# Kernel optimization log

Measured on AMD Instinct MI355X. Metric: run time of the kernel, lower is better.

## Reference

```python
import jax, jax.numpy as jnp
import numpy as np

EPS = 1e-5  # BatchNorm eps


def _bn_relu(x, g, b, m, v):
    # inference-mode BatchNorm2d over channel axis 1, then ReLU
    inv = g / jnp.sqrt(v + EPS)
    return jax.nn.relu(x * inv[None, :, None, None] + (b - m * inv)[None, :, None, None])


def setup_inputs() -> dict:
    key = jax.random.key(0)
    ks = jax.random.split(key, 16)
    B, C, N, K = 8, 64, 16384, 16
    mlp = (128, 64, 64)
    inp = {
        "src_xyz": jax.random.normal(ks[0], (B, 3, N, K), jnp.float32),
        "tgt_xyz": jax.random.normal(ks[1], (B, 3, N), jnp.float32),
        "feature": jax.random.normal(ks[2], (B, C, N, K), jnp.float32),
    }
    prev = C + 4  # use_relation adds diff_xyz(3) + distance(1)
    i = 3
    for li, co in enumerate(mlp, 1):
        scale = (6.0 / (prev + co)) ** 0.5  # xavier_uniform
        inp[f"W{li}"] = jax.random.uniform(ks[i], (co, prev), jnp.float32, -scale, scale)
        inp[f"g{li}"] = jnp.ones((co,), jnp.float32)
        inp[f"b{li}"] = jnp.zeros((co,), jnp.float32)
        inp[f"m{li}"] = jnp.zeros((co,), jnp.float32)
        inp[f"v{li}"] = jnp.ones((co,), jnp.float32)
        prev = co
        i += 1
    return inp


def reference(src_xyz, tgt_xyz, feature,
              W1, g1, b1, m1, v1,
              W2, g2, b2, m2, v2,
              W3, g3, b3, m3, v3):
    d = 3  # NOTE: original code slices the NEIGHBOR dim to :3 (faithful quirk)
    diff = src_xyz[:, :, :, :d] - tgt_xyz[:, :, :, None]      # (B,3,N,3)
    dist = jnp.sum(diff * diff, axis=1, keepdims=True)        # (B,1,N,3)
    x = jnp.concatenate([feature[:, :, :, :d], diff, dist], axis=1)  # (B,C+4,N,3)
    for (W, g, b, m, v) in ((W1, g1, b1, m1, v1), (W2, g2, b2, m2, v2), (W3, g3, b3, m3, v3)):
        x = jnp.einsum('oc,bcnk->bonk', W, x)  # 1x1 conv (shared MLP)
        x = _bn_relu(x, g, b, m, v)
    return jnp.sum(x, axis=3)  # reduction='sum' over neighbor dim -> (B,64,N)
```

## Files before the change

kernel.cpp:

```cpp
#include <hip/hip_runtime.h>


typedef __attribute__((ext_vector_type(8))) short short8v;
typedef __attribute__((ext_vector_type(4))) float f32x4;

#define BN_EPS 1e-5f

__device__ __forceinline__ unsigned short f2bf(float f) {
    union { float f; unsigned u; } U; U.f = f;
    unsigned r = U.u + 0x7FFFu + ((U.u >> 16) & 1u);
    return (unsigned short)(r >> 16);
}

union FragU { uint4 u; short8v s; uint2 h[2]; };


__global__ __launch_bounds__(256) void fa_pack(
    const float* __restrict__ W1, const float* __restrict__ g1, const float* __restrict__ b1,
    const float* __restrict__ m1, const float* __restrict__ v1,
    const float* __restrict__ W2, const float* __restrict__ g2, const float* __restrict__ b2,
    const float* __restrict__ m2, const float* __restrict__ v2,
    const float* __restrict__ W3, const float* __restrict__ g3, const float* __restrict__ b3,
    const float* __restrict__ m3, const float* __restrict__ v3,
    char* __restrict__ ws)
{
    const int id = blockIdx.x * 256 + threadIdx.x;
    if (id < 1536) {
        const int lane = id & 63, frag = id >> 6;
        const int ct = frag / 3, ks = frag - 3 * ct;
        const int o  = ct * 16 + (lane & 15);
        const int kb = ks * 32 + (lane >> 4) * 8;
        unsigned short h[8];
        #pragma unroll
        for (int j = 0; j < 8; ++j) {
            const int k = kb + j;
            h[j] = (k < 68) ? f2bf(W1[o * 68 + k]) : (unsigned short)0;
        }
        uint4 pk;
        pk.x = h[0] | (h[1] << 16); pk.y = h[2] | (h[3] << 16);
        pk.z = h[4] | (h[5] << 16); pk.w = h[6] | (h[7] << 16);
        ((uint4*)ws)[id] = pk;
    } else if (id < 2560) {
        const int i2 = id - 1536;
        const int lane = i2 & 63, frag = i2 >> 6;
        const int o  = (frag >> 2) * 16 + (lane & 15);
        const int kb = (frag & 3) * 32 + (lane >> 4) * 8;
        unsigned short h[8];
        #pragma unroll
        for (int j = 0; j < 8; ++j) h[j] = f2bf(W2[o * 128 + kb + j]);
        uint4 pk;
        pk.x = h[0] | (h[1] << 16); pk.y = h[2] | (h[3] << 16);
        pk.z = h[4] | (h[5] << 16); pk.w = h[6] | (h[7] << 16);
        ((uint4*)(ws + 24576))[i2] = pk;
    } else if (id < 3072) {
        const int i3 = id - 2560;
        const int lane = i3 & 63, frag = i3 >> 6;
        const int o  = (frag >> 1) * 16 + (lane & 15);
        const int kb = (frag & 1) * 32 + (lane >> 4) * 8;
        unsigned short h[8];
        #pragma unroll
        for (int j = 0; j < 8; ++j) h[j] = f2bf(W3[o * 64 + kb + j]);
        uint4 pk;
        pk.x = h[0] | (h[1] << 16); pk.y = h[2] | (h[3] << 16);
        pk.z = h[4] | (h[5] << 16); pk.w = h[6] | (h[7] << 16);
        ((uint4*)(ws + 40960))[i3] = pk;
    } else if (id < 3200) {
        const int o = id - 3072;
        const float s = g1[o] * rsqrtf(v1[o] + BN_EPS);
        ((float*)(ws + 49152))[o] = s;
        ((float*)(ws + 49664))[o] = b1[o] - m1[o] * s;
    } else if (id < 3264) {
        const int o = id - 3200;
        const float s = g2[o] * rsqrtf(v2[o] + BN_EPS);
        ((float*)(ws + 50176))[o] = s;
        ((float*)(ws + 50432))[o] = b2[o] - m2[o] * s;
    } else if (id < 3328) {
        const int o = id - 3264;
        const float s = g3[o] * rsqrtf(v3[o] + BN_EPS);
        ((float*)(ws + 50688))[o] = s;
        ((float*)(ws + 50944))[o] = b3[o] - m3[o] * s;
    }
}

__global__ __launch_bounds__(128, 3) void fa_mfma(
    const float* __restrict__ src, const float* __restrict__ tgt,
    const float* __restrict__ feat,
    const char* __restrict__ ws, float* __restrict__ out)
{
    constexpr int N = 16384;
    __shared__ unsigned short SM[96 * 136];
    #define X0V(r, c) SM[(r) * 72 + (c)]
    #define X1V(r, c) SM[(r) * 136 + (c)]

    const int t  = threadIdx.x;
    const int b  = blockIdx.x >> 9;
    const int n0 = (blockIdx.x & 511) << 5;

    {
        const int p  = t & 31;
        const int cg = t >> 5;
        float4 fr[16];
        #pragma unroll
        for (int it = 0; it < 4; ++it) {
            const float* fp = feat + ((size_t)(b * 64 + it * 16 + cg * 4) * N + n0 + p) * 16;
            #pragma unroll
            for (int q = 0; q < 4; ++q)
                fr[it * 4 + q] = *(const float4*)(fp + (size_t)q * N * 16);
        }
        float rs0 = 0, rs1 = 0, rs2 = 0, rt0 = 0, rt1 = 0, rt2 = 0;
        const bool rel = t < 96;
        const int rp = t & 31, rk = t >> 5;
        if (rel) {
            const int n = n0 + rp;
            rs0 = src[((b * 3 + 0) * N + n) * 16 + rk]; rt0 = tgt[(b * 3 + 0) * N + n];
            rs1 = src[((b * 3 + 1) * N + n) * 16 + rk]; rt1 = tgt[(b * 3 + 1) * N + n];
            rs2 = src[((b * 3 + 2) * N + n) * 16 + rk]; rt2 = tgt[(b * 3 + 2) * N + n];
        }
        #pragma unroll
        for (int it = 0; it < 4; ++it) {
            const int c0 = it * 16 + cg * 4;
            const float4 f0 = fr[it * 4 + 0], f1 = fr[it * 4 + 1];
            const float4 f2 = fr[it * 4 + 2], f3 = fr[it * 4 + 3];
            uint2 u0, u1, u2;
            u0.x = f2bf(f0.x) | (f2bf(f1.x) << 16); u0.y = f2bf(f2.x) | (f2bf(f3.x) << 16);
            u1.x = f2bf(f0.y) | (f2bf(f1.y) << 16); u1.y = f2bf(f2.y) | (f2bf(f3.y) << 16);
            u2.x = f2bf(f0.z) | (f2bf(f1.z) << 16); u2.y = f2bf(f2.z) | (f2bf(f3.z) << 16);
            *(uint2*)&X0V(0 * 32 + p, c0) = u0;
            *(uint2*)&X0V(1 * 32 + p, c0) = u1;
            *(uint2*)&X0V(2 * 32 + p, c0) = u2;
        }
        if (rel) {
            const float d0 = rs0 - rt0, d1 = rs1 - rt1, d2 = rs2 - rt2;
            const float ds = d0 * d0 + d1 * d1 + d2 * d2;
            uint2 wr; wr.x = f2bf(d0) | (f2bf(d1) << 16); wr.y = f2bf(d2) | (f2bf(ds) << 16);
            *(uint2*)&X0V(rk * 32 + rp, 64) = wr;
        }
    }
    __syncthreads();

    const int w = t >> 6, lane = t & 63, lo = lane & 15, hi = lane >> 4;

    const uint4*  w1f = (const uint4*)ws;
    const uint4*  w2f = (const uint4*)(ws + 24576);
    const uint4*  w3f = (const uint4*)(ws + 40960);
    const float*  s1w = (const float*)(ws + 49152);
    const float*  t1w = (const float*)(ws + 49664);
    const float*  s2w = (const float*)(ws + 50176);
    const float*  t2w = (const float*)(ws + 50432);
    const float*  s3w = (const float*)(ws + 50688);
    const float*  t3w = (const float*)(ws + 50944);

    short8v a1[3][3];
    #pragma unroll
    for (int k = 0; k < 3; ++k) {
        const int row = k * 32 + w * 16 + lo;
        a1[k][0] = *(const short8v*)&X0V(row, hi * 8);
        a1[k][1] = *(const short8v*)&X0V(row, 32 + hi * 8);
        FragU U; U.u.x = 0; U.u.y = 0; U.u.z = 0; U.u.w = 0;
        if (hi == 0) U.h[0] = *(const uint2*)&X0V(row, 64);
        a1[k][2] = U.s;
    }
    __syncthreads();

    #pragma unroll 2
    for (int ct = 0; ct < 8; ++ct) {
        FragU B0, B1, B2;
        B0.u = w1f[(ct * 3 + 0) * 64 + lane];
        B1.u = w1f[(ct * 3 + 1) * 64 + lane];
        B2.u = w1f[(ct * 3 + 2) * 64 + lane];
        const float sc = s1w[ct * 16 + lo];
        const float tb = t1w[ct * 16 + lo];
        #pragma unroll
        for (int k = 0; k < 3; ++k) {
            f32x4 acc = {0.f, 0.f, 0.f, 0.f};
            acc = __builtin_amdgcn_mfma_f32_16x16x32_bf16(a1[k][0], B0.s, acc, 0, 0, 0);
            acc = __builtin_amdgcn_mfma_f32_16x16x32_bf16(a1[k][1], B1.s, acc, 0, 0, 0);
            acc = __builtin_amdgcn_mfma_f32_16x16x32_bf16(a1[k][2], B2.s, acc, 0, 0, 0);
            const int rb = k * 32 + w * 16 + 4 * hi;
            #pragma unroll
            for (int j = 0; j < 4; ++j) {
                const float y = fmaxf(fmaf(sc, acc[j], tb), 0.f);
                X1V(rb + j, ct * 16 + lo) = f2bf(y);
            }
        }
    }

    short8v a2[3][4];
    #pragma unroll
    for (int k = 0; k < 3; ++k) {
        const int row = k * 32 + w * 16 + lo;
        #pragma unroll
        for (int ks = 0; ks < 4; ++ks)
            a2[k][ks] = *(const short8v*)&X1V(row, ks * 32 + hi * 8);
    }
    __syncthreads();

    #pragma unroll 2
    for (int ct = 0; ct < 4; ++ct) {
        FragU B0, B1, B2, B3;
        B0.u = w2f[(ct * 4 + 0) * 64 + lane];
        B1.u = w2f[(ct * 4 + 1) * 64 + lane];
        B2.u = w2f[(ct * 4 + 2) * 64 + lane];
        B3.u = w2f[(ct * 4 + 3) * 64 + lane];
        const float sc = s2w[ct * 16 + lo];
        const float tb = t2w[ct * 16 + lo];
        #pragma unroll
        for (int k = 0; k < 3; ++k) {
            f32x4 acc = {0.f, 0.f, 0.f, 0.f};
            acc = __builtin_amdgcn_mfma_f32_16x16x32_bf16(a2[k][0], B0.s, acc, 0, 0, 0);
            acc = __builtin_amdgcn_mfma_f32_16x16x32_bf16(a2[k][1], B1.s, acc, 0, 0, 0);
            acc = __builtin_amdgcn_mfma_f32_16x16x32_bf16(a2[k][2], B2.s, acc, 0, 0, 0);
            acc = __builtin_amdgcn_mfma_f32_16x16x32_bf16(a2[k][3], B3.s, acc, 0, 0, 0);
            const int rb = k * 32 + w * 16 + 4 * hi;
            #pragma unroll
            for (int j = 0; j < 4; ++j) {
                const float y = fmaxf(fmaf(sc, acc[j], tb), 0.f);
                X0V(rb + j, ct * 16 + lo) = f2bf(y);
            }
        }
    }

    short8v a3[3][2];
    #pragma unroll
    for (int k = 0; k < 3; ++k) {
        const int row = k * 32 + w * 16 + lo;
        a3[k][0] = *(const short8v*)&X0V(row, hi * 8);
        a3[k][1] = *(const short8v*)&X0V(row, 32 + hi * 8);
    }
    #pragma unroll 2
    for (int ct = 0; ct < 4; ++ct) {
        FragU B0, B1;
        B0.u = w3f[(ct * 2 + 0) * 64 + lane];
        B1.u = w3f[(ct * 2 + 1) * 64 + lane];
        const float sc = s3w[ct * 16 + lo];
        const float tb = t3w[ct * 16 + lo];
        f32x4 acc0 = {0.f, 0.f, 0.f, 0.f};
        f32x4 acc1 = {0.f, 0.f, 0.f, 0.f};
        f32x4 acc2 = {0.f, 0.f, 0.f, 0.f};
        acc0 = __builtin_amdgcn_mfma_f32_16x16x32_bf16(a3[0][0], B0.s, acc0, 0, 0, 0);
        acc0 = __builtin_amdgcn_mfma_f32_16x16x32_bf16(a3[0][1], B1.s, acc0, 0, 0, 0);
        acc1 = __builtin_amdgcn_mfma_f32_16x16x32_bf16(a3[1][0], B0.s, acc1, 0, 0, 0);
        acc1 = __builtin_amdgcn_mfma_f32_16x16x32_bf16(a3[1][1], B1.s, acc1, 0, 0, 0);
        acc2 = __builtin_amdgcn_mfma_f32_16x16x32_bf16(a3[2][0], B0.s, acc2, 0, 0, 0);
        acc2 = __builtin_amdgcn_mfma_f32_16x16x32_bf16(a3[2][1], B1.s, acc2, 0, 0, 0);
        float4 r;
        float* rp = &r.x;
        #pragma unroll
        for (int j = 0; j < 4; ++j) {
            rp[j] = fmaxf(fmaf(sc, acc0[j], tb), 0.f)
                  + fmaxf(fmaf(sc, acc1[j], tb), 0.f)
                  + fmaxf(fmaf(sc, acc2[j], tb), 0.f);
        }
        float* op = out + (size_t)(b * 64 + ct * 16 + lo) * N + n0 + w * 16 + 4 * hi;
        *(float4*)op = r;
    }
    #undef X0V
    #undef X1V
}

extern "C" void kernel_launch(void* const* d_in, const int* in_sizes, int n_in,
                              void* d_out, int out_size, void* d_ws, size_t ws_size,
                              hipStream_t stream)
{
    const float* src  = (const float*)d_in[0];
    const float* tgt  = (const float*)d_in[1];
    const float* feat = (const float*)d_in[2];
    const float* W1 = (const float*)d_in[3];
    const float* g1 = (const float*)d_in[4];
    const float* b1 = (const float*)d_in[5];
    const float* m1 = (const float*)d_in[6];
    const float* v1 = (const float*)d_in[7];
    const float* W2 = (const float*)d_in[8];
    const float* g2 = (const float*)d_in[9];
    const float* b2 = (const float*)d_in[10];
    const float* m2 = (const float*)d_in[11];
    const float* v2 = (const float*)d_in[12];
    const float* W3 = (const float*)d_in[13];
    const float* g3 = (const float*)d_in[14];
    const float* b3 = (const float*)d_in[15];
    const float* m3 = (const float*)d_in[16];
    const float* v3 = (const float*)d_in[17];
    float* out = (float*)d_out;
    char* ws = (char*)d_ws;

    hipLaunchKernelGGL(fa_pack, dim3(13), dim3(256), 0, stream,
                       W1, g1, b1, m1, v1, W2, g2, b2, m2, v2, W3, g3, b3, m3, v3, ws);
    hipLaunchKernelGGL(fa_mfma, dim3(8 * 512), dim3(128), 0, stream,
                       src, tgt, feat, ws, out);
}
```

Baseline: 136.7 us.

## Process two tiles per block and prefetch the second tile's inputs during MLP compute

Each block now handles two consecutive 32-point tiles and launches half as many blocks. The global loads of feature, src and tgt for the second tile are issued while layers 1 and 2 of the first tile run, then packed into bf16 and written to shared memory after the first tile's layer-3 fragments are read. This is meant to hide global memory latency behind MFMA work. In exchange it uses more registers for the prefetch buffers, which may hurt occupancy under the launch bound of 3, and it halves the grid size.

```diff
diff --git a/kernel.cpp b/kernel.cpp
--- a/kernel.cpp
+++ b/kernel.cpp
@@ -93,28 +93,44 @@
     #define X1V(r, c) SM[(r) * 136 + (c)]
 
     const int t  = threadIdx.x;
-    const int b  = blockIdx.x >> 9;
-    const int n0 = (blockIdx.x & 511) << 5;
+    const int T0 = blockIdx.x * 2;
+    const int b0  = T0 >> 9;
+    const int n00 = (T0 & 511) << 5;
+    const int b1t  = (T0 + 1) >> 9;
+    const int n01 = ((T0 + 1) & 511) << 5;
+
+    const int p  = t & 31;
+    const int cg = t >> 5;
+    const bool rel = t < 96;
+    const int rp = t & 31, rk = t >> 5;
+
+    const int w = t >> 6, lane = t & 63, lo = lane & 15, hi = lane >> 4;
+
+    const uint4*  w1f = (const uint4*)ws;
+    const uint4*  w2f = (const uint4*)(ws + 24576);
+    const uint4*  w3f = (const uint4*)(ws + 40960);
+    const float*  s1w = (const float*)(ws + 49152);
+    const float*  t1w = (const float*)(ws + 49664);
+    const float*  s2w = (const float*)(ws + 50176);
+    const float*  t2w = (const float*)(ws + 50432);
+    const float*  s3w = (const float*)(ws + 50688);
+    const float*  t3w = (const float*)(ws + 50944);
 
     {
-        const int p  = t & 31;
-        const int cg = t >> 5;
         float4 fr[16];
         #pragma unroll
         for (int it = 0; it < 4; ++it) {
-            const float* fp = feat + ((size_t)(b * 64 + it * 16 + cg * 4) * N + n0 + p) * 16;
+            const float* fp = feat + ((size_t)(b0 * 64 + it * 16 + cg * 4) * N + n00 + p) * 16;
             #pragma unroll
             for (int q = 0; q < 4; ++q)
                 fr[it * 4 + q] = *(const float4*)(fp + (size_t)q * N * 16);
         }
         float rs0 = 0, rs1 = 0, rs2 = 0, rt0 = 0, rt1 = 0, rt2 = 0;
-        const bool rel = t < 96;
-        const int rp = t & 31, rk = t >> 5;
         if (rel) {
-            const int n = n0 + rp;
-            rs0 = src[((b * 3 + 0) * N + n) * 16 + rk]; rt0 = tgt[(b * 3 + 0) * N + n];
-            rs1 = src[((b * 3 + 1) * N + n) * 16 + rk]; rt1 = tgt[(b * 3 + 1) * N + n];
-            rs2 = src[((b * 3 + 2) * N + n) * 16 + rk]; rt2 = tgt[(b * 3 + 2) * N + n];
+            const int n = n00 + rp;
+            rs0 = src[((b0 * 3 + 0) * N + n) * 16 + rk]; rt0 = tgt[(b0 * 3 + 0) * N + n];
+            rs1 = src[((b0 * 3 + 1) * N + n) * 16 + rk]; rt1 = tgt[(b0 * 3 + 1) * N + n];
+            rs2 = src[((b0 * 3 + 2) * N + n) * 16 + rk]; rt2 = tgt[(b0 * 3 + 2) * N + n];
         }
         #pragma unroll
         for (int it = 0; it < 4; ++it) {
@@ -138,18 +154,6 @@
     }
     __syncthreads();
 
-    const int w = t >> 6, lane = t & 63, lo = lane & 15, hi = lane >> 4;
-
-    const uint4*  w1f = (const uint4*)ws;
-    const uint4*  w2f = (const uint4*)(ws + 24576);
-    const uint4*  w3f = (const uint4*)(ws + 40960);
-    const float*  s1w = (const float*)(ws + 49152);
-    const float*  t1w = (const float*)(ws + 49664);
-    const float*  s2w = (const float*)(ws + 50176);
-    const float*  t2w = (const float*)(ws + 50432);
-    const float*  s3w = (const float*)(ws + 50688);
-    const float*  t3w = (const float*)(ws + 50944);
-
     short8v a1[3][3];
     #pragma unroll
     for (int k = 0; k < 3; ++k) {
@@ -161,6 +165,22 @@
         a1[k][2] = U.s;
     }
     __syncthreads();
+
+    float4 frA[8];
+    #pragma unroll
+    for (int it = 0; it < 2; ++it) {
+        const float* fp = feat + ((size_t)(b1t * 64 + it * 16 + cg * 4) * N + n01 + p) * 16;
+        #pragma unroll
+        for (int q = 0; q < 4; ++q)
+            frA[it * 4 + q] = *(const float4*)(fp + (size_t)q * N * 16);
+    }
+    float prs0 = 0, prs1 = 0, prs2 = 0, prt0 = 0, prt1 = 0, prt2 = 0;
+    if (rel) {
+        const int n = n01 + rp;
+        prs0 = src[((b1t * 3 + 0) * N + n) * 16 + rk]; prt0 = tgt[(b1t * 3 + 0) * N + n];
+        prs1 = src[((b1t * 3 + 1) * N + n) * 16 + rk]; prt1 = tgt[(b1t * 3 + 1) * N + n];
+        prs2 = src[((b1t * 3 + 2) * N + n) * 16 + rk]; prt2 = tgt[(b1t * 3 + 2) * N + n];
+    }
 
     #pragma unroll 2
     for (int ct = 0; ct < 8; ++ct) {
@@ -183,6 +203,27 @@
                 X1V(rb + j, ct * 16 + lo) = f2bf(y);
             }
         }
+    }
+
+    uint2 pk[12];
+    #pragma unroll
+    for (int it = 0; it < 2; ++it) {
+        const float4 f0 = frA[it * 4 + 0], f1 = frA[it * 4 + 1];
+        const float4 f2 = frA[it * 4 + 2], f3 = frA[it * 4 + 3];
+        pk[it * 3 + 0].x = f2bf(f0.x) | (f2bf(f1.x) << 16);
+        pk[it * 3 + 0].y = f2bf(f2.x) | (f2bf(f3.x) << 16);
+        pk[it * 3 + 1].x = f2bf(f0.y) | (f2bf(f1.y) << 16);
+        pk[it * 3 + 1].y = f2bf(f2.y) | (f2bf(f3.y) << 16);
+        pk[it * 3 + 2].x = f2bf(f0.z) | (f2bf(f1.z) << 16);
+        pk[it * 3 + 2].y = f2bf(f2.z) | (f2bf(f3.z) << 16);
+    }
+    float4 frB[8];
+    #pragma unroll
+    for (int it = 0; it < 2; ++it) {
+        const float* fp = feat + ((size_t)(b1t * 64 + (it + 2) * 16 + cg * 4) * N + n01 + p) * 16;
+        #pragma unroll
+        for (int q = 0; q < 4; ++q)
+            frB[it * 4 + q] = *(const float4*)(fp + (size_t)q * N * 16);
     }
 
     short8v a2[3][4];
@@ -220,6 +261,18 @@
         }
     }
 
+    #pragma unroll
+    for (int it = 0; it < 2; ++it) {
+        const float4 f0 = frB[it * 4 + 0], f1 = frB[it * 4 + 1];
+        const float4 f2 = frB[it * 4 + 2], f3 = frB[it * 4 + 3];
+        pk[6 + it * 3 + 0].x = f2bf(f0.x) | (f2bf(f1.x) << 16);
+        pk[6 + it * 3 + 0].y = f2bf(f2.x) | (f2bf(f3.x) << 16);
+        pk[6 + it * 3 + 1].x = f2bf(f0.y) | (f2bf(f1.y) << 16);
+        pk[6 + it * 3 + 1].y = f2bf(f2.y) | (f2bf(f3.y) << 16);
+        pk[6 + it * 3 + 2].x = f2bf(f0.z) | (f2bf(f1.z) << 16);
+        pk[6 + it * 3 + 2].y = f2bf(f2.z) | (f2bf(f3.z) << 16);
+    }
+
     short8v a3[3][2];
     #pragma unroll
     for (int k = 0; k < 3; ++k) {
@@ -227,6 +280,22 @@
         a3[k][0] = *(const short8v*)&X0V(row, hi * 8);
         a3[k][1] = *(const short8v*)&X0V(row, 32 + hi * 8);
     }
+    __syncthreads();
+
+    #pragma unroll
+    for (int it = 0; it < 4; ++it) {
+        const int c0 = it * 16 + cg * 4;
+        *(uint2*)&X0V(0 * 32 + p, c0) = pk[it * 3 + 0];
+        *(uint2*)&X0V(1 * 32 + p, c0) = pk[it * 3 + 1];
+        *(uint2*)&X0V(2 * 32 + p, c0) = pk[it * 3 + 2];
+    }
+    if (rel) {
+        const float d0 = prs0 - prt0, d1 = prs1 - prt1, d2 = prs2 - prt2;
+        const float ds = d0 * d0 + d1 * d1 + d2 * d2;
+        uint2 wr; wr.x = f2bf(d0) | (f2bf(d1) << 16); wr.y = f2bf(d2) | (f2bf(ds) << 16);
+        *(uint2*)&X0V(rk * 32 + rp, 64) = wr;
+    }
+
     #pragma unroll 2
     for (int ct = 0; ct < 4; ++ct) {
         FragU B0, B1;
@@ -244,14 +313,117 @@
         acc2 = __builtin_amdgcn_mfma_f32_16x16x32_bf16(a3[2][0], B0.s, acc2, 0, 0, 0);
         acc2 = __builtin_amdgcn_mfma_f32_16x16x32_bf16(a3[2][1], B1.s, acc2, 0, 0, 0);
         float4 r;
-        float* rp = &r.x;
+        float* rp4 = &r.x;
         #pragma unroll
         for (int j = 0; j < 4; ++j) {
-            rp[j] = fmaxf(fmaf(sc, acc0[j], tb), 0.f)
-                  + fmaxf(fmaf(sc, acc1[j], tb), 0.f)
-                  + fmaxf(fmaf(sc, acc2[j], tb), 0.f);
-        }
-        float* op = out + (size_t)(b * 64 + ct * 16 + lo) * N + n0 + w * 16 + 4 * hi;
+            rp4[j] = fmaxf(fmaf(sc, acc0[j], tb), 0.f)
+                   + fmaxf(fmaf(sc, acc1[j], tb), 0.f)
+                   + fmaxf(fmaf(sc, acc2[j], tb), 0.f);
+        }
+        float* op = out + (size_t)(b0 * 64 + ct * 16 + lo) * N + n00 + w * 16 + 4 * hi;
+        *(float4*)op = r;
+    }
+    __syncthreads();
+
+    #pragma unroll
+    for (int k = 0; k < 3; ++k) {
+        const int row = k * 32 + w * 16 + lo;
+        a1[k][0] = *(const short8v*)&X0V(row, hi * 8);
+        a1[k][1] = *(const short8v*)&X0V(row, 32 + hi * 8);
+        FragU U; U.u.x = 0; U.u.y = 0; U.u.z = 0; U.u.w = 0;
+        if (hi == 0) U.h[0] = *(const uint2*)&X0V(row, 64);
+        a1[k][2] = U.s;
+    }
+    __syncthreads();
+
+    #pragma unroll 2
+    for (int ct = 0; ct < 8; ++ct) {
+        FragU B0, B1, B2;
+        B0.u = w1f[(ct * 3 + 0) * 64 + lane];
+        B1.u = w1f[(ct * 3 + 1) * 64 + lane];
+        B2.u = w1f[(ct * 3 + 2) * 64 + lane];
+        const float sc = s1w[ct * 16 + lo];
+        const float tb = t1w[ct * 16 + lo];
+        #pragma unroll
+        for (int k = 0; k < 3; ++k) {
+            f32x4 acc = {0.f, 0.f, 0.f, 0.f};
+            acc = __builtin_amdgcn_mfma_f32_16x16x32_bf16(a1[k][0], B0.s, acc, 0, 0, 0);
+            acc = __builtin_amdgcn_mfma_f32_16x16x32_bf16(a1[k][1], B1.s, acc, 0, 0, 0);
+            acc = __builtin_amdgcn_mfma_f32_16x16x32_bf16(a1[k][2], B2.s, acc, 0, 0, 0);
+            const int rb = k * 32 + w * 16 + 4 * hi;
+            #pragma unroll
+            for (int j = 0; j < 4; ++j) {
+                const float y = fmaxf(fmaf(sc, acc[j], tb), 0.f);
+                X1V(rb + j, ct * 16 + lo) = f2bf(y);
+            }
+        }
+    }
+
+    #pragma unroll
+    for (int k = 0; k < 3; ++k) {
+        const int row = k * 32 + w * 16 + lo;
+        #pragma unroll
+        for (int ks = 0; ks < 4; ++ks)
+            a2[k][ks] = *(const short8v*)&X1V(row, ks * 32 + hi * 8);
+    }
+    __syncthreads();
+
+    #pragma unroll 2
+    for (int ct = 0; ct < 4; ++ct) {
+        FragU B0, B1, B2, B3;
+        B0.u = w2f[(ct * 4 + 0) * 64 + lane];
+        B1.u = w2f[(ct * 4 + 1) * 64 + lane];
+        B2.u = w2f[(ct * 4 + 2) * 64 + lane];
+        B3.u = w2f[(ct * 4 + 3) * 64 + lane];
+        const float sc = s2w[ct * 16 + lo];
+        const float tb = t2w[ct * 16 + lo];
+        #pragma unroll
+        for (int k = 0; k < 3; ++k) {
+            f32x4 acc = {0.f, 0.f, 0.f, 0.f};
+            acc = __builtin_amdgcn_mfma_f32_16x16x32_bf16(a2[k][0], B0.s, acc, 0, 0, 0);
+            acc = __builtin_amdgcn_mfma_f32_16x16x32_bf16(a2[k][1], B1.s, acc, 0, 0, 0);
+            acc = __builtin_amdgcn_mfma_f32_16x16x32_bf16(a2[k][2], B2.s, acc, 0, 0, 0);
+            acc = __builtin_amdgcn_mfma_f32_16x16x32_bf16(a2[k][3], B3.s, acc, 0, 0, 0);
+            const int rb = k * 32 + w * 16 + 4 * hi;
+            #pragma unroll
+            for (int j = 0; j < 4; ++j) {
+                const float y = fmaxf(fmaf(sc, acc[j], tb), 0.f);
+                X0V(rb + j, ct * 16 + lo) = f2bf(y);
+            }
+        }
+    }
+
+    #pragma unroll
+    for (int k = 0; k < 3; ++k) {
+        const int row = k * 32 + w * 16 + lo;
+        a3[k][0] = *(const short8v*)&X0V(row, hi * 8);
+        a3[k][1] = *(const short8v*)&X0V(row, 32 + hi * 8);
+    }
+    #pragma unroll 2
+    for (int ct = 0; ct < 4; ++ct) {
+        FragU B0, B1;
+        B0.u = w3f[(ct * 2 + 0) * 64 + lane];
+        B1.u = w3f[(ct * 2 + 1) * 64 + lane];
+        const float sc = s3w[ct * 16 + lo];
+        const float tb = t3w[ct * 16 + lo];
+        f32x4 acc0 = {0.f, 0.f, 0.f, 0.f};
+        f32x4 acc1 = {0.f, 0.f, 0.f, 0.f};
+        f32x4 acc2 = {0.f, 0.f, 0.f, 0.f};
+        acc0 = __builtin_amdgcn_mfma_f32_16x16x32_bf16(a3[0][0], B0.s, acc0, 0, 0, 0);
+        acc0 = __builtin_amdgcn_mfma_f32_16x16x32_bf16(a3[0][1], B1.s, acc0, 0, 0, 0);
+        acc1 = __builtin_amdgcn_mfma_f32_16x16x32_bf16(a3[1][0], B0.s, acc1, 0, 0, 0);
+        acc1 = __builtin_amdgcn_mfma_f32_16x16x32_bf16(a3[1][1], B1.s, acc1, 0, 0, 0);
+        acc2 = __builtin_amdgcn_mfma_f32_16x16x32_bf16(a3[2][0], B0.s, acc2, 0, 0, 0);
+        acc2 = __builtin_amdgcn_mfma_f32_16x16x32_bf16(a3[2][1], B1.s, acc2, 0, 0, 0);
+        float4 r;
+        float* rp4 = &r.x;
+        #pragma unroll
+        for (int j = 0; j < 4; ++j) {
+            rp4[j] = fmaxf(fmaf(sc, acc0[j], tb), 0.f)
+                   + fmaxf(fmaf(sc, acc1[j], tb), 0.f)
+                   + fmaxf(fmaf(sc, acc2[j], tb), 0.f);
+        }
+        float* op = out + (size_t)(b1t * 64 + ct * 16 + lo) * N + n01 + w * 16 + 4 * hi;
         *(float4*)op = r;
     }
     #undef X0V
@@ -285,6 +457,6 @@
 
     hipLaunchKernelGGL(fa_pack, dim3(13), dim3(256), 0, stream,
                        W1, g1, b1, m1, v1, W2, g2, b2, m2, v2, W3, g3, b3, m3, v3, ws);
-    hipLaunchKernelGGL(fa_mfma, dim3(8 * 512), dim3(128), 0, stream,
+    hipLaunchKernelGGL(fa_mfma, dim3(2048), dim3(128), 0, stream,
                        src, tgt, feat, ws, out);
 }
```

Result: slower. 154.3 us (+12.8%).

## Use single-wave blocks with LDS fences instead of block barriers

Applied to the files above, without the earlier changes.

Shrinks each block to a single 64-lane wave handling 16 points, so the __syncthreads barriers become s_waitcnt lgkmcnt fences wrapped in sched_barriers. Layer 1 is restructured to run per neighbor slice into a smaller 16-row staging buffer, which cuts LDS per block. The aim is to drop barrier cost and allow more resident blocks. The trade-offs are twice as many blocks, and each wave now reloads the layer-1 weights three times.

```diff
diff --git a/kernel.cpp b/kernel.cpp
--- a/kernel.cpp
+++ b/kernel.cpp
@@ -5,6 +5,12 @@
 typedef __attribute__((ext_vector_type(4))) float f32x4;
 
 #define BN_EPS 1e-5f
+
+#define LDS_FENCE() do {                                        \
+    __builtin_amdgcn_sched_barrier(0);                          \
+    asm volatile("s_waitcnt lgkmcnt(0)" ::: "memory");          \
+    __builtin_amdgcn_sched_barrier(0);                          \
+} while (0)
 
 __device__ __forceinline__ unsigned short f2bf(float f) {
     union { float f; unsigned u; } U; U.f = f;
@@ -82,34 +88,34 @@
     }
 }
 
-__global__ __launch_bounds__(128, 3) void fa_mfma(
+__global__ __launch_bounds__(64, 3) void fa_mfma(
     const float* __restrict__ src, const float* __restrict__ tgt,
     const float* __restrict__ feat,
     const char* __restrict__ ws, float* __restrict__ out)
 {
     constexpr int N = 16384;
-    __shared__ unsigned short SM[96 * 136];
-    #define X0V(r, c) SM[(r) * 72 + (c)]
-    #define X1V(r, c) SM[(r) * 136 + (c)]
+    __shared__ unsigned short X0[48 * 72];
+    __shared__ unsigned short Y[16 * 136];
 
     const int t  = threadIdx.x;
-    const int b  = blockIdx.x >> 9;
-    const int n0 = (blockIdx.x & 511) << 5;
+    const int b  = blockIdx.x >> 10;
+    const int n0 = (blockIdx.x & 1023) << 4;
+
+    const int p  = t & 15;
+    const int cs = t >> 4;
 
     {
-        const int p  = t & 31;
-        const int cg = t >> 5;
         float4 fr[16];
         #pragma unroll
         for (int it = 0; it < 4; ++it) {
-            const float* fp = feat + ((size_t)(b * 64 + it * 16 + cg * 4) * N + n0 + p) * 16;
+            const float* fp = feat + ((size_t)(b * 64 + it * 16 + cs * 4) * N + n0 + p) * 16;
             #pragma unroll
             for (int q = 0; q < 4; ++q)
                 fr[it * 4 + q] = *(const float4*)(fp + (size_t)q * N * 16);
         }
         float rs0 = 0, rs1 = 0, rs2 = 0, rt0 = 0, rt1 = 0, rt2 = 0;
-        const bool rel = t < 96;
-        const int rp = t & 31, rk = t >> 5;
+        const bool rel = t < 48;
+        const int rp = t & 15, rk = t >> 4;
         if (rel) {
             const int n = n0 + rp;
             rs0 = src[((b * 3 + 0) * N + n) * 16 + rk]; rt0 = tgt[(b * 3 + 0) * N + n];
@@ -118,27 +124,27 @@
         }
         #pragma unroll
         for (int it = 0; it < 4; ++it) {
-            const int c0 = it * 16 + cg * 4;
+            const int c0 = it * 16 + cs * 4;
             const float4 f0 = fr[it * 4 + 0], f1 = fr[it * 4 + 1];
             const float4 f2 = fr[it * 4 + 2], f3 = fr[it * 4 + 3];
             uint2 u0, u1, u2;
             u0.x = f2bf(f0.x) | (f2bf(f1.x) << 16); u0.y = f2bf(f2.x) | (f2bf(f3.x) << 16);
             u1.x = f2bf(f0.y) | (f2bf(f1.y) << 16); u1.y = f2bf(f2.y) | (f2bf(f3.y) << 16);
             u2.x = f2bf(f0.z) | (f2bf(f1.z) << 16); u2.y = f2bf(f2.z) | (f2bf(f3.z) << 16);
-            *(uint2*)&X0V(0 * 32 + p, c0) = u0;
-            *(uint2*)&X0V(1 * 32 + p, c0) = u1;
-            *(uint2*)&X0V(2 * 32 + p, c0) = u2;
+            *(uint2*)&X0[(0 * 16 + p) * 72 + c0] = u0;
+            *(uint2*)&X0[(1 * 16 + p) * 72 + c0] = u1;
+            *(uint2*)&X0[(2 * 16 + p) * 72 + c0] = u2;
         }
         if (rel) {
             const float d0 = rs0 - rt0, d1 = rs1 - rt1, d2 = rs2 - rt2;
             const float ds = d0 * d0 + d1 * d1 + d2 * d2;
             uint2 wr; wr.x = f2bf(d0) | (f2bf(d1) << 16); wr.y = f2bf(d2) | (f2bf(ds) << 16);
-            *(uint2*)&X0V(rk * 32 + rp, 64) = wr;
-        }
-    }
-    __syncthreads();
-
-    const int w = t >> 6, lane = t & 63, lo = lane & 15, hi = lane >> 4;
+            *(uint2*)&X0[(rk * 16 + rp) * 72 + 64] = wr;
+        }
+    }
+    LDS_FENCE();
+
+    const int lo = t & 15, hi = t >> 4;
 
     const uint4*  w1f = (const uint4*)ws;
     const uint4*  w2f = (const uint4*)(ws + 24576);
@@ -150,58 +156,50 @@
     const float*  s3w = (const float*)(ws + 50688);
     const float*  t3w = (const float*)(ws + 50944);
 
-    short8v a1[3][3];
+    short8v a2[3][4];
     #pragma unroll
     for (int k = 0; k < 3; ++k) {
-        const int row = k * 32 + w * 16 + lo;
-        a1[k][0] = *(const short8v*)&X0V(row, hi * 8);
-        a1[k][1] = *(const short8v*)&X0V(row, 32 + hi * 8);
-        FragU U; U.u.x = 0; U.u.y = 0; U.u.z = 0; U.u.w = 0;
-        if (hi == 0) U.h[0] = *(const uint2*)&X0V(row, 64);
-        a1[k][2] = U.s;
-    }
-    __syncthreads();
-
-    #pragma unroll 2
-    for (int ct = 0; ct < 8; ++ct) {
-        FragU B0, B1, B2;
-        B0.u = w1f[(ct * 3 + 0) * 64 + lane];
-        B1.u = w1f[(ct * 3 + 1) * 64 + lane];
-        B2.u = w1f[(ct * 3 + 2) * 64 + lane];
-        const float sc = s1w[ct * 16 + lo];
-        const float tb = t1w[ct * 16 + lo];
-        #pragma unroll
-        for (int k = 0; k < 3; ++k) {
+        const int row = k * 16 + lo;
+        const short8v a10 = *(const short8v*)&X0[row * 72 + hi * 8];
+        const short8v a11 = *(const short8v*)&X0[row * 72 + 32 + hi * 8];
+        short8v a12;
+        {
+            FragU U; U.u.x = 0; U.u.y = 0; U.u.z = 0; U.u.w = 0;
+            if (hi == 0) U.h[0] = *(const uint2*)&X0[row * 72 + 64];
+            a12 = U.s;
+        }
+        #pragma unroll 2
+        for (int ct = 0; ct < 8; ++ct) {
+            FragU B0, B1, B2;
+            B0.u = w1f[(ct * 3 + 0) * 64 + t];
+            B1.u = w1f[(ct * 3 + 1) * 64 + t];
+            B2.u = w1f[(ct * 3 + 2) * 64 + t];
+            const float sc = s1w[ct * 16 + lo];
+            const float tb = t1w[ct * 16 + lo];
             f32x4 acc = {0.f, 0.f, 0.f, 0.f};
-            acc = __builtin_amdgcn_mfma_f32_16x16x32_bf16(a1[k][0], B0.s, acc, 0, 0, 0);
-            acc = __builtin_amdgcn_mfma_f32_16x16x32_bf16(a1[k][1], B1.s, acc, 0, 0, 0);
-            acc = __builtin_amdgcn_mfma_f32_16x16x32_bf16(a1[k][2], B2.s, acc, 0, 0, 0);
-            const int rb = k * 32 + w * 16 + 4 * hi;
+            acc = __builtin_amdgcn_mfma_f32_16x16x32_bf16(a10, B0.s, acc, 0, 0, 0);
+            acc = __builtin_amdgcn_mfma_f32_16x16x32_bf16(a11, B1.s, acc, 0, 0, 0);
+            acc = __builtin_amdgcn_mfma_f32_16x16x32_bf16(a12, B2.s, acc, 0, 0, 0);
             #pragma unroll
             for (int j = 0; j < 4; ++j) {
                 const float y = fmaxf(fmaf(sc, acc[j], tb), 0.f);
-                X1V(rb + j, ct * 16 + lo) = f2bf(y);
+                Y[(4 * hi + j) * 136 + ct * 16 + lo] = f2bf(y);
             }
         }
-    }
-
-    short8v a2[3][4];
-    #pragma unroll
-    for (int k = 0; k < 3; ++k) {
-        const int row = k * 32 + w * 16 + lo;
+        LDS_FENCE();
         #pragma unroll
         for (int ks = 0; ks < 4; ++ks)
-            a2[k][ks] = *(const short8v*)&X1V(row, ks * 32 + hi * 8);
-    }
-    __syncthreads();
+            a2[k][ks] = *(const short8v*)&Y[lo * 136 + ks * 32 + hi * 8];
+        LDS_FENCE();
+    }
 
     #pragma unroll 2
     for (int ct = 0; ct < 4; ++ct) {
         FragU B0, B1, B2, B3;
-        B0.u = w2f[(ct * 4 + 0) * 64 + lane];
-        B1.u = w2f[(ct * 4 + 1) * 64 + lane];
-        B2.u = w2f[(ct * 4 + 2) * 64 + lane];
-        B3.u = w2f[(ct * 4 + 3) * 64 + lane];
+        B0.u = w2f[(ct * 4 + 0) * 64 + t];
+        B1.u = w2f[(ct * 4 + 1) * 64 + t];
+        B2.u = w2f[(ct * 4 + 2) * 64 + t];
+        B3.u = w2f[(ct * 4 + 3) * 64 + t];
         const float sc = s2w[ct * 16 + lo];
         const float tb = t2w[ct * 16 + lo];
         #pragma unroll
@@ -211,27 +209,28 @@
             acc = __builtin_amdgcn_mfma_f32_16x16x32_bf16(a2[k][1], B1.s, acc, 0, 0, 0);
             acc = __builtin_amdgcn_mfma_f32_16x16x32_bf16(a2[k][2], B2.s, acc, 0, 0, 0);
             acc = __builtin_amdgcn_mfma_f32_16x16x32_bf16(a2[k][3], B3.s, acc, 0, 0, 0);
-            const int rb = k * 32 + w * 16 + 4 * hi;
+            const int rb = k * 16 + 4 * hi;
             #pragma unroll
             for (int j = 0; j < 4; ++j) {
                 const float y = fmaxf(fmaf(sc, acc[j], tb), 0.f);
-                X0V(rb + j, ct * 16 + lo) = f2bf(y);
+                X0[(rb + j) * 72 + ct * 16 + lo] = f2bf(y);
             }
         }
     }
+    LDS_FENCE();
 
     short8v a3[3][2];
     #pragma unroll
     for (int k = 0; k < 3; ++k) {
-        const int row = k * 32 + w * 16 + lo;
-        a3[k][0] = *(const short8v*)&X0V(row, hi * 8);
-        a3[k][1] = *(const short8v*)&X0V(row, 32 + hi * 8);
+        const int row = k * 16 + lo;
+        a3[k][0] = *(const short8v*)&X0[row * 72 + hi * 8];
+        a3[k][1] = *(const short8v*)&X0[row * 72 + 32 + hi * 8];
     }
     #pragma unroll 2
     for (int ct = 0; ct < 4; ++ct) {
         FragU B0, B1;
-        B0.u = w3f[(ct * 2 + 0) * 64 + lane];
-        B1.u = w3f[(ct * 2 + 1) * 64 + lane];
+        B0.u = w3f[(ct * 2 + 0) * 64 + t];
+        B1.u = w3f[(ct * 2 + 1) * 64 + t];
         const float sc = s3w[ct * 16 + lo];
         const float tb = t3w[ct * 16 + lo];
         f32x4 acc0 = {0.f, 0.f, 0.f, 0.f};
@@ -244,18 +243,16 @@
         acc2 = __builtin_amdgcn_mfma_f32_16x16x32_bf16(a3[2][0], B0.s, acc2, 0, 0, 0);
         acc2 = __builtin_amdgcn_mfma_f32_16x16x32_bf16(a3[2][1], B1.s, acc2, 0, 0, 0);
         float4 r;
-        float* rp = &r.x;
+        float* rp4 = &r.x;
         #pragma unroll
         for (int j = 0; j < 4; ++j) {
-            rp[j] = fmaxf(fmaf(sc, acc0[j], tb), 0.f)
-                  + fmaxf(fmaf(sc, acc1[j], tb), 0.f)
-                  + fmaxf(fmaf(sc, acc2[j], tb), 0.f);
-        }
-        float* op = out + (size_t)(b * 64 + ct * 16 + lo) * N + n0 + w * 16 + 4 * hi;
+            rp4[j] = fmaxf(fmaf(sc, acc0[j], tb), 0.f)
+                   + fmaxf(fmaf(sc, acc1[j], tb), 0.f)
+                   + fmaxf(fmaf(sc, acc2[j], tb), 0.f);
+        }
+        float* op = out + (size_t)(b * 64 + ct * 16 + lo) * N + n0 + 4 * hi;
         *(float4*)op = r;
     }
-    #undef X0V
-    #undef X1V
 }
 
 extern "C" void kernel_launch(void* const* d_in, const int* in_sizes, int n_in,
@@ -285,6 +282,6 @@
 
     hipLaunchKernelGGL(fa_pack, dim3(13), dim3(256), 0, stream,
                        W1, g1, b1, m1, v1, W2, g2, b2, m2, v2, W3, g3, b3, m3, v3, ws);
-    hipLaunchKernelGGL(fa_mfma, dim3(8 * 512), dim3(128), 0, stream,
+    hipLaunchKernelGGL(fa_mfma, dim3(8 * 1024), dim3(64), 0, stream,
                        src, tgt, feat, ws, out);
 }
```

New measurement: 141.1 us. +3.2%, slower.

## Make blocks persistent over four point tiles with async global-to-LDS prefetch

Applied to the files above, without the earlier changes.

Each block now handles four consecutive 32-point tiles instead of one, so the grid drops from 4096 to 1024 blocks. The next tile's feature data is prefetched straight into LDS with global_load_lds while the layer-2 and layer-3 MFMAs of the current tile run, and the relation inputs are loaded into registers at the same point. This aims to hide global-memory latency behind compute. In exchange it adds a 24 KB staging buffer, lowers the occupancy hint from 3 to 2 blocks, and performs only 3 of the 16 neighbor floats per channel per load instead of full float4 reads.

```diff
diff --git a/kernel.cpp b/kernel.cpp
--- a/kernel.cpp
+++ b/kernel.cpp
@@ -82,63 +82,25 @@
     }
 }
 
-__global__ __launch_bounds__(128, 3) void fa_mfma(
+__global__ __launch_bounds__(128, 2) void fa_mfma(
     const float* __restrict__ src, const float* __restrict__ tgt,
     const float* __restrict__ feat,
     const char* __restrict__ ws, float* __restrict__ out)
 {
     constexpr int N = 16384;
     __shared__ unsigned short SM[96 * 136];
+    __shared__ float RAW[32 * 192];
     #define X0V(r, c) SM[(r) * 72 + (c)]
     #define X1V(r, c) SM[(r) * 136 + (c)]
 
-    const int t  = threadIdx.x;
-    const int b  = blockIdx.x >> 9;
-    const int n0 = (blockIdx.x & 511) << 5;
-
-    {
-        const int p  = t & 31;
-        const int cg = t >> 5;
-        float4 fr[16];
-        #pragma unroll
-        for (int it = 0; it < 4; ++it) {
-            const float* fp = feat + ((size_t)(b * 64 + it * 16 + cg * 4) * N + n0 + p) * 16;
-            #pragma unroll
-            for (int q = 0; q < 4; ++q)
-                fr[it * 4 + q] = *(const float4*)(fp + (size_t)q * N * 16);
-        }
-        float rs0 = 0, rs1 = 0, rs2 = 0, rt0 = 0, rt1 = 0, rt2 = 0;
-        const bool rel = t < 96;
-        const int rp = t & 31, rk = t >> 5;
-        if (rel) {
-            const int n = n0 + rp;
-            rs0 = src[((b * 3 + 0) * N + n) * 16 + rk]; rt0 = tgt[(b * 3 + 0) * N + n];
-            rs1 = src[((b * 3 + 1) * N + n) * 16 + rk]; rt1 = tgt[(b * 3 + 1) * N + n];
-            rs2 = src[((b * 3 + 2) * N + n) * 16 + rk]; rt2 = tgt[(b * 3 + 2) * N + n];
-        }
-        #pragma unroll
-        for (int it = 0; it < 4; ++it) {
-            const int c0 = it * 16 + cg * 4;
-            const float4 f0 = fr[it * 4 + 0], f1 = fr[it * 4 + 1];
-            const float4 f2 = fr[it * 4 + 2], f3 = fr[it * 4 + 3];
-            uint2 u0, u1, u2;
-            u0.x = f2bf(f0.x) | (f2bf(f1.x) << 16); u0.y = f2bf(f2.x) | (f2bf(f3.x) << 16);
-            u1.x = f2bf(f0.y) | (f2bf(f1.y) << 16); u1.y = f2bf(f2.y) | (f2bf(f3.y) << 16);
-            u2.x = f2bf(f0.z) | (f2bf(f1.z) << 16); u2.y = f2bf(f2.z) | (f2bf(f3.z) << 16);
-            *(uint2*)&X0V(0 * 32 + p, c0) = u0;
-            *(uint2*)&X0V(1 * 32 + p, c0) = u1;
-            *(uint2*)&X0V(2 * 32 + p, c0) = u2;
-        }
-        if (rel) {
-            const float d0 = rs0 - rt0, d1 = rs1 - rt1, d2 = rs2 - rt2;
-            const float ds = d0 * d0 + d1 * d1 + d2 * d2;
-            uint2 wr; wr.x = f2bf(d0) | (f2bf(d1) << 16); wr.y = f2bf(d2) | (f2bf(ds) << 16);
-            *(uint2*)&X0V(rk * 32 + rp, 64) = wr;
-        }
-    }
-    __syncthreads();
+    const int t = threadIdx.x;
+    const int b      = blockIdx.x >> 7;
+    const int base_n = (blockIdx.x & 127) << 7;
 
     const int w = t >> 6, lane = t & 63, lo = lane & 15, hi = lane >> 4;
+    const int p32 = t & 31, cg = t >> 5;
+    const bool rel = t < 96;
+    const int rp = t & 31, rk = t >> 5;
 
     const uint4*  w1f = (const uint4*)ws;
     const uint4*  w2f = (const uint4*)(ws + 24576);
@@ -150,109 +112,182 @@
     const float*  s3w = (const float*)(ws + 50688);
     const float*  t3w = (const float*)(ws + 50944);
 
-    short8v a1[3][3];
-    #pragma unroll
-    for (int k = 0; k < 3; ++k) {
-        const int row = k * 32 + w * 16 + lo;
-        a1[k][0] = *(const short8v*)&X0V(row, hi * 8);
-        a1[k][1] = *(const short8v*)&X0V(row, 32 + hi * 8);
-        FragU U; U.u.x = 0; U.u.y = 0; U.u.z = 0; U.u.w = 0;
-        if (hi == 0) U.h[0] = *(const uint2*)&X0V(row, 64);
-        a1[k][2] = U.s;
-    }
-    __syncthreads();
-
-    #pragma unroll 2
-    for (int ct = 0; ct < 8; ++ct) {
-        FragU B0, B1, B2;
-        B0.u = w1f[(ct * 3 + 0) * 64 + lane];
-        B1.u = w1f[(ct * 3 + 1) * 64 + lane];
-        B2.u = w1f[(ct * 3 + 2) * 64 + lane];
-        const float sc = s1w[ct * 16 + lo];
-        const float tb = t1w[ct * 16 + lo];
+    auto stage_async = [&](int n0s) {
+        #pragma unroll
+        for (int i = 0; i < 16; ++i) {
+            const int c = w * 32 + i * 2 + (lane >> 5);
+            const float* gsrc = feat + ((size_t)(b * 64 + c) * N + n0s + (lane & 31)) * 16;
+            float* lbase = &RAW[(size_t)(w * 16 + i) * 192];
+            __builtin_amdgcn_global_load_lds(
+                (const __attribute__((address_space(1))) void*)(gsrc + 0),
+                (__attribute__((address_space(3))) void*)(lbase + 0), 4, 0, 0);
+            __builtin_amdgcn_global_load_lds(
+                (const __attribute__((address_space(1))) void*)(gsrc + 1),
+                (__attribute__((address_space(3))) void*)(lbase + 64), 4, 0, 0);
+            __builtin_amdgcn_global_load_lds(
+                (const __attribute__((address_space(1))) void*)(gsrc + 2),
+                (__attribute__((address_space(3))) void*)(lbase + 128), 4, 0, 0);
+        }
+    };
+
+    float q0 = 0, q1 = 0, q2 = 0, q3 = 0, q4 = 0, q5 = 0;
+    auto rel_load = [&](int n0s) {
+        if (rel) {
+            const int n = n0s + rp;
+            q0 = src[((b * 3 + 0) * N + n) * 16 + rk]; q3 = tgt[(b * 3 + 0) * N + n];
+            q1 = src[((b * 3 + 1) * N + n) * 16 + rk]; q4 = tgt[(b * 3 + 1) * N + n];
+            q2 = src[((b * 3 + 2) * N + n) * 16 + rk]; q5 = tgt[(b * 3 + 2) * N + n];
+        }
+    };
+
+    stage_async(base_n);
+    rel_load(base_n);
+
+    #pragma unroll 1
+    for (int tt = 0; tt < 4; ++tt) {
+        const int n0 = base_n + tt * 32;
+
+        asm volatile("s_waitcnt vmcnt(0)" ::: "memory");
+        __builtin_amdgcn_sched_barrier(0);
+        __syncthreads();
+
+        #pragma unroll
+        for (int j2 = 0; j2 < 4; ++j2) {
+            const int c0 = cg * 16 + 4 * j2;
+            float f[4][3];
+            #pragma unroll
+            for (int q = 0; q < 4; ++q) {
+                const int c = c0 + q;
+                const int base = (c >> 1) * 192 + (c & 1) * 32 + p32;
+                f[q][0] = RAW[base];
+                f[q][1] = RAW[base + 64];
+                f[q][2] = RAW[base + 128];
+            }
+            uint2 u0, u1, u2;
+            u0.x = f2bf(f[0][0]) | (f2bf(f[1][0]) << 16); u0.y = f2bf(f[2][0]) | (f2bf(f[3][0]) << 16);
+            u1.x = f2bf(f[0][1]) | (f2bf(f[1][1]) << 16); u1.y = f2bf(f[2][1]) | (f2bf(f[3][1]) << 16);
+            u2.x = f2bf(f[0][2]) | (f2bf(f[1][2]) << 16); u2.y = f2bf(f[2][2]) | (f2bf(f[3][2]) << 16);
+            *(uint2*)&X0V(0 * 32 + p32, c0) = u0;
+            *(uint2*)&X0V(1 * 32 + p32, c0) = u1;
+            *(uint2*)&X0V(2 * 32 + p32, c0) = u2;
+        }
+        if (rel) {
+            const float d0 = q0 - q3, d1 = q1 - q4, d2 = q2 - q5;
+            const float ds = d0 * d0 + d1 * d1 + d2 * d2;
+            uint2 wr; wr.x = f2bf(d0) | (f2bf(d1) << 16); wr.y = f2bf(d2) | (f2bf(ds) << 16);
+            *(uint2*)&X0V(rk * 32 + rp, 64) = wr;
+        }
+        __syncthreads();
+
+        short8v a1[3][3];
         #pragma unroll
         for (int k = 0; k < 3; ++k) {
-            f32x4 acc = {0.f, 0.f, 0.f, 0.f};
-            acc = __builtin_amdgcn_mfma_f32_16x16x32_bf16(a1[k][0], B0.s, acc, 0, 0, 0);
-            acc = __builtin_amdgcn_mfma_f32_16x16x32_bf16(a1[k][1], B1.s, acc, 0, 0, 0);
-            acc = __builtin_amdgcn_mfma_f32_16x16x32_bf16(a1[k][2], B2.s, acc, 0, 0, 0);
-            const int rb = k * 32 + w * 16 + 4 * hi;
+            const int row = k * 32 + w * 16 + lo;
+            a1[k][0] = *(const short8v*)&X0V(row, hi * 8);
+            a1[k][1] = *(const short8v*)&X0V(row, 32 + hi * 8);
+            FragU U; U.u.x = 0; U.u.y = 0; U.u.z = 0; U.u.w = 0;
+            if (hi == 0) U.h[0] = *(const uint2*)&X0V(row, 64);
+            a1[k][2] = U.s;
+        }
+        __syncthreads();
+
+        #pragma unroll 2
+        for (int ct = 0; ct < 8; ++ct) {
+            FragU B0, B1, B2;
+            B0.u = w1f[(ct * 3 + 0) * 64 + lane];
+            B1.u = w1f[(ct * 3 + 1) * 64 + lane];
+            B2.u = w1f[(ct * 3 + 2) * 64 + lane];
+            const float sc = s1w[ct * 16 + lo];
+            const float tb = t1w[ct * 16 + lo];
+            #pragma unroll
+            for (int k = 0; k < 3; ++k) {
+                f32x4 acc = {0.f, 0.f, 0.f, 0.f};
+                acc = __builtin_amdgcn_mfma_f32_16x16x32_bf16(a1[k][0], B0.s, acc, 0, 0, 0);
+                acc = __builtin_amdgcn_mfma_f32_16x16x32_bf16(a1[k][1], B1.s, acc, 0, 0, 0);
+                acc = __builtin_amdgcn_mfma_f32_16x16x32_bf16(a1[k][2], B2.s, acc, 0, 0, 0);
+                const int rb = k * 32 + w * 16 + 4 * hi;
+                #pragma unroll
+                for (int j = 0; j < 4; ++j) {
+                    const float y = fmaxf(fmaf(sc, acc[j], tb), 0.f);
+                    X1V(rb + j, ct * 16 + lo) = f2bf(y);
+                }
+            }
+        }
+
+        short8v a2[3][4];
+        #pragma unroll
+        for (int k = 0; k < 3; ++k) {
+            const int row = k * 32 + w * 16 + lo;
+            #pragma unroll
+            for (int ks = 0; ks < 4; ++ks)
+                a2[k][ks] = *(const short8v*)&X1V(row, ks * 32 + hi * 8);
+        }
+        __syncthreads();
+
+        if (tt < 3) {
+            stage_async(n0 + 32);
+            rel_load(n0 + 32);
+        }
+
+        #pragma unroll 2
+        for (int ct = 0; ct < 4; ++ct) {
+            FragU B0, B1, B2, B3;
+            B0.u = w2f[(ct * 4 + 0) * 64 + lane];
+            B1.u = w2f[(ct * 4 + 1) * 64 + lane];
+            B2.u = w2f[(ct * 4 + 2) * 64 + lane];
+            B3.u = w2f[(ct * 4 + 3) * 64 + lane];
+            const float sc = s2w[ct * 16 + lo];
+            const float tb = t2w[ct * 16 + lo];
+            #pragma unroll
+            for (int k = 0; k < 3; ++k) {
+                f32x4 acc = {0.f, 0.f, 0.f, 0.f};
+                acc = __builtin_amdgcn_mfma_f32_16x16x32_bf16(a2[k][0], B0.s, acc, 0, 0, 0);
+                acc = __builtin_amdgcn_mfma_f32_16x16x32_bf16(a2[k][1], B1.s, acc, 0, 0, 0);
+                acc = __builtin_amdgcn_mfma_f32_16x16x32_bf16(a2[k][2], B2.s, acc, 0, 0, 0);
+                acc = __builtin_amdgcn_mfma_f32_16x16x32_bf16(a2[k][3], B3.s, acc, 0, 0, 0);
+                const int rb = k * 32 + w * 16 + 4 * hi;
+                #pragma unroll
+                for (int j = 0; j < 4; ++j) {
+                    const float y = fmaxf(fmaf(sc, acc[j], tb), 0.f);
+                    X0V(rb + j, ct * 16 + lo) = f2bf(y);
+                }
+            }
+        }
+
+        short8v a3[3][2];
+        #pragma unroll
+        for (int k = 0; k < 3; ++k) {
+            const int row = k * 32 + w * 16 + lo;
+            a3[k][0] = *(const short8v*)&X0V(row, hi * 8);
+            a3[k][1] = *(const short8v*)&X0V(row, 32 + hi * 8);
+        }
+        #pragma unroll 2
+        for (int ct = 0; ct < 4; ++ct) {
+            FragU B0, B1;
+            B0.u = w3f[(ct * 2 + 0) * 64 + lane];
+            B1.u = w3f[(ct * 2 + 1) * 64 + lane];
+            const float sc = s3w[ct * 16 + lo];
+            const float tb = t3w[ct * 16 + lo];
+            f32x4 acc0 = {0.f, 0.f, 0.f, 0.f};
+            f32x4 acc1 = {0.f, 0.f, 0.f, 0.f};
+            f32x4 acc2 = {0.f, 0.f, 0.f, 0.f};
+            acc0 = __builtin_amdgcn_mfma_f32_16x16x32_bf16(a3[0][0], B0.s, acc0, 0, 0, 0);
+            acc0 = __builtin_amdgcn_mfma_f32_16x16x32_bf16(a3[0][1], B1.s, acc0, 0, 0, 0);
+            acc1 = __builtin_amdgcn_mfma_f32_16x16x32_bf16(a3[1][0], B0.s, acc1, 0, 0, 0);
+            acc1 = __builtin_amdgcn_mfma_f32_16x16x32_bf16(a3[1][1], B1.s, acc1, 0, 0, 0);
+            acc2 = __builtin_amdgcn_mfma_f32_16x16x32_bf16(a3[2][0], B0.s, acc2, 0, 0, 0);
+            acc2 = __builtin_amdgcn_mfma_f32_16x16x32_bf16(a3[2][1], B1.s, acc2, 0, 0, 0);
+            float4 r;
+            float* rp4 = &r.x;
             #pragma unroll
             for (int j = 0; j < 4; ++j) {
-                const float y = fmaxf(fmaf(sc, acc[j], tb), 0.f);
-                X1V(rb + j, ct * 16 + lo) = f2bf(y);
+                rp4[j] = fmaxf(fmaf(sc, acc0[j], tb), 0.f)
+                       + fmaxf(fmaf(sc, acc1[j], tb), 0.f)
+                       + fmaxf(fmaf(sc, acc2[j], tb), 0.f);
             }
-        }
-    }
-
-    short8v a2[3][4];
-    #pragma unroll
-    for (int k = 0; k < 3; ++k) {
-        const int row = k * 32 + w * 16 + lo;
-        #pragma unroll
-        for (int ks = 0; ks < 4; ++ks)
-            a2[k][ks] = *(const short8v*)&X1V(row, ks * 32 + hi * 8);
-    }
-    __syncthreads();
-
-    #pragma unroll 2
-    for (int ct = 0; ct < 4; ++ct) {
-        FragU B0, B1, B2, B3;
-        B0.u = w2f[(ct * 4 + 0) * 64 + lane];
-        B1.u = w2f[(ct * 4 + 1) * 64 + lane];
-        B2.u = w2f[(ct * 4 + 2) * 64 + lane];
-        B3.u = w2f[(ct * 4 + 3) * 64 + lane];
-        const float sc = s2w[ct * 16 + lo];
-        const float tb = t2w[ct * 16 + lo];
-        #pragma unroll
-        for (int k = 0; k < 3; ++k) {
-            f32x4 acc = {0.f, 0.f, 0.f, 0.f};
-            acc = __builtin_amdgcn_mfma_f32_16x16x32_bf16(a2[k][0], B0.s, acc, 0, 0, 0);
-            acc = __builtin_amdgcn_mfma_f32_16x16x32_bf16(a2[k][1], B1.s, acc, 0, 0, 0);
-            acc = __builtin_amdgcn_mfma_f32_16x16x32_bf16(a2[k][2], B2.s, acc, 0, 0, 0);
-            acc = __builtin_amdgcn_mfma_f32_16x16x32_bf16(a2[k][3], B3.s, acc, 0, 0, 0);
-            const int rb = k * 32 + w * 16 + 4 * hi;
-            #pragma unroll
-            for (int j = 0; j < 4; ++j) {
-                const float y = fmaxf(fmaf(sc, acc[j], tb), 0.f);
-                X0V(rb + j, ct * 16 + lo) = f2bf(y);
-            }
-        }
-    }
-
-    short8v a3[3][2];
-    #pragma unroll
-    for (int k = 0; k < 3; ++k) {
-        const int row = k * 32 + w * 16 + lo;
-        a3[k][0] = *(const short8v*)&X0V(row, hi * 8);
-        a3[k][1] = *(const short8v*)&X0V(row, 32 + hi * 8);
-    }
-    #pragma unroll 2
-    for (int ct = 0; ct < 4; ++ct) {
-        FragU B0, B1;
-        B0.u = w3f[(ct * 2 + 0) * 64 + lane];
-        B1.u = w3f[(ct * 2 + 1) * 64 + lane];
-        const float sc = s3w[ct * 16 + lo];
-        const float tb = t3w[ct * 16 + lo];
-        f32x4 acc0 = {0.f, 0.f, 0.f, 0.f};
-        f32x4 acc1 = {0.f, 0.f, 0.f, 0.f};
-        f32x4 acc2 = {0.f, 0.f, 0.f, 0.f};
-        acc0 = __builtin_amdgcn_mfma_f32_16x16x32_bf16(a3[0][0], B0.s, acc0, 0, 0, 0);
-        acc0 = __builtin_amdgcn_mfma_f32_16x16x32_bf16(a3[0][1], B1.s, acc0, 0, 0, 0);
-        acc1 = __builtin_amdgcn_mfma_f32_16x16x32_bf16(a3[1][0], B0.s, acc1, 0, 0, 0);
-        acc1 = __builtin_amdgcn_mfma_f32_16x16x32_bf16(a3[1][1], B1.s, acc1, 0, 0, 0);
-        acc2 = __builtin_amdgcn_mfma_f32_16x16x32_bf16(a3[2][0], B0.s, acc2, 0, 0, 0);
-        acc2 = __builtin_amdgcn_mfma_f32_16x16x32_bf16(a3[2][1], B1.s, acc2, 0, 0, 0);
-        float4 r;
-        float* rp = &r.x;
-        #pragma unroll
-        for (int j = 0; j < 4; ++j) {
-            rp[j] = fmaxf(fmaf(sc, acc0[j], tb), 0.f)
-                  + fmaxf(fmaf(sc, acc1[j], tb), 0.f)
-                  + fmaxf(fmaf(sc, acc2[j], tb), 0.f);
-        }
-        float* op = out + (size_t)(b * 64 + ct * 16 + lo) * N + n0 + w * 16 + 4 * hi;
-        *(float4*)op = r;
+            float* op = out + (size_t)(b * 64 + ct * 16 + lo) * N + n0 + w * 16 + 4 * hi;
+            *(float4*)op = r;
+        }
     }
     #undef X0V
     #undef X1V
@@ -285,6 +320,6 @@
 
     hipLaunchKernelGGL(fa_pack, dim3(13), dim3(256), 0, stream,
                        W1, g1, b1, m1, v1, W2, g2, b2, m2, v2, W3, g3, b3, m3, v3, ws);
-    hipLaunchKernelGGL(fa_mfma, dim3(8 * 512), dim3(128), 0, stream,
+    hipLaunchKernelGGL(fa_mfma, dim3(1024), dim3(128), 0, stream,
                        src, tgt, feat, ws, out);
 }
```

After: 199.6 us. 1.46x slower.
